# Optimization experiments

Hardware: AMD Instinct MI355X
Metric: run time of the kernel (lower is better)

The kernel has to match this reference:

```python
import jax, jax.numpy as jnp
import numpy as np
from jax import lax

GAMMA = 1.0
BIG = 1e8  # matches the torch init value 100000000.0


def setup_inputs() -> dict:
    key = jax.random.key(0)
    k1, k2 = jax.random.split(key)
    B, n, m, d = 256, 256, 256, 32
    x = jax.random.normal(k1, (B, n, d), dtype=jnp.float32)
    y = jax.random.normal(k2, (B, m, d), dtype=jnp.float32)
    return {"x": x, "y": y}


def _soft_dtw(x, y, gamma):
    B, n, d = x.shape
    m = y.shape[1]
    # squared euclidean distances, (B, n, m); GEMM form avoids the (B,n,m,d) blowup
    x2 = jnp.sum(x * x, axis=-1)
    y2 = jnp.sum(y * y, axis=-1)
    dist = x2[:, :, None] + y2[:, None, :] - 2.0 * jnp.einsum('bnd,bmd->bnm', x, y)
    dist = jnp.maximum(dist, 0.0)  # cdist(p=2)**2 is nonnegative

    def softmin3(a, b, c):
        s = jnp.stack([a, b, c], axis=0)
        return -gamma * jax.nn.logsumexp(-s / gamma, axis=0)

    big_col = jnp.full((B,), BIG, dtype=x.dtype)

    def row_step(prev_row, d_row):
        # prev_row: (B, m+1) = D[i-1, :];  d_row: (B, m) = dist[:, i-1, :]
        def col_step(cur, inp):
            # cur: (B,) = D[i, j-1]; inp: (dist[i-1,j-1], D[i-1,j], D[i-1,j-1])
            dij, up, diag = inp
            new = dij + softmin3(up, cur, diag)
            return new, new
        xs = (d_row.T, prev_row[:, 1:].T, prev_row[:, :-1].T)  # each (m, B)
        _, vals = lax.scan(col_step, big_col, xs)  # vals: (m, B)
        new_row = jnp.concatenate([big_col[:, None], vals.T], axis=1)  # (B, m+1)
        return new_row, None

    init_row = jnp.concatenate(
        [jnp.zeros((B, 1), x.dtype), jnp.full((B, m), BIG, dtype=x.dtype)], axis=1)
    final_row, _ = lax.scan(row_step, init_row, jnp.swapaxes(dist, 0, 1))  # scan over n rows
    return jnp.mean(final_row[:, m])


def reference(x, y):
    return _soft_dtw(x, y, GAMMA)
```

## Files before the change

### kernel.cpp

```cpp
#include <hip/hip_runtime.h>

#define BIG 1e8f
#define LN2 0.69314718f
#define LOG2E 1.44269504f
#define M2L -2.8853900818f

#define RSLOT 112
#define DRB 1040

#define OFF_XH   116480
#define OFF_X2S  132864
#define OFF_Y2S  133888
#define OFF_RDY  134912
#define OFF_PRG  134976
#define LDS_BYTES 135040

typedef _Float16 half8 __attribute__((ext_vector_type(8)));
typedef _Float16 half2_t __attribute__((ext_vector_type(2)));
typedef float f32x4 __attribute__((ext_vector_type(4)));

__device__ __forceinline__ float exp2g(float x) {
#if __has_builtin(__builtin_amdgcn_exp2f)
    return __builtin_amdgcn_exp2f(x);
#else
    return exp2f(x);
#endif
}
__device__ __forceinline__ float log2g(float x) {
#if __has_builtin(__builtin_amdgcn_logf)
    return __builtin_amdgcn_logf(x);
#else
    return log2f(x);
#endif
}

__device__ __forceinline__ half2_t pkrtz(float a, float b) {
    return __builtin_bit_cast(half2_t, __builtin_amdgcn_cvt_pkrtz(a, b));
}

__device__ __forceinline__ void pairp(float a, float b, float& m, float& s) {
    m = fminf(a, b);
    s = exp2g(-fabsf(a - b)) + 1.f;
}
__device__ __forceinline__ float smp(float m, float s, float v) {
    float d = v - m;
    float t = exp2g(-fabsf(d));
    float r = (d > 0.f) ? (t + s) : fmaf(s, t, 1.f);
    return fminf(m, v) - log2g(r);
}

__device__ __forceinline__ float shfl_up1(float v, float oldv) {
    int r = __builtin_amdgcn_update_dpp(
        __builtin_bit_cast(int, oldv), __builtin_bit_cast(int, v),
        0x138 , 0xf, 0xf, false);
    return __builtin_bit_cast(float, r);
}

__device__ __forceinline__ void dec2(unsigned int w, float& a, float& b) {
    half2_t h = __builtin_bit_cast(half2_t, w);
    a = (float)h[0];
    b = (float)h[1];
}

__global__ __launch_bounds__(128, 1) void sdtw_kernel(
    const float* __restrict__ x, const float* __restrict__ y,
    float* __restrict__ out) {
    extern __shared__ __align__(16) char smem[];
    unsigned char* band = (unsigned char*)smem;
    _Float16* xh = (_Float16*)(smem + OFF_XH);
    float* x2sL = (float*)(smem + OFF_X2S);
    float* y2sL = (float*)(smem + OFF_Y2S);
    volatile int* rdy = (volatile int*)(smem + OFF_RDY);
    volatile int* prg = (volatile int*)(smem + OFF_PRG);

    const int tid = threadIdx.x;
    const int b = blockIdx.x;
    const float* xb = x + (size_t)b * 8192;
    const float* yb = y + (size_t)b * 8192;

#pragma unroll
    for (int rr = 0; rr < 2; rr++) {
        const int r = tid + rr * 128;
        const float4* px = (const float4*)(xb + r * 32);
        union { _Float16 h[32]; half8 v[4]; } uc;
        float s2 = 0.f;
#pragma unroll
        for (int q = 0; q < 8; q++) {
            float4 f = px[q];
            s2 += f.x * f.x + f.y * f.y + f.z * f.z + f.w * f.w;
            uc.h[4 * q + 0] = (_Float16)f.x;
            uc.h[4 * q + 1] = (_Float16)f.y;
            uc.h[4 * q + 2] = (_Float16)f.z;
            uc.h[4 * q + 3] = (_Float16)f.w;
        }
        half8* dst = (half8*)&xh[r * 32];
#pragma unroll
        for (int q = 0; q < 4; q++) dst[q] = uc.v[q];
        x2sL[r] = s2 * LOG2E;

        const float4* py = (const float4*)(yb + r * 32);
        float t2 = 0.f;
#pragma unroll
        for (int q = 0; q < 8; q++) {
            float4 f = py[q];
            t2 += f.x * f.x + f.y * f.y + f.z * f.z + f.w * f.w;
        }
        y2sL[r] = t2 * LOG2E;
    }
    if (tid < 16) rdy[tid] = 0;
    if (tid == 16) *prg = 0;
    __syncthreads();

    if (tid >= 64) {
        const int lane = tid - 64;
        const int qd = lane >> 4, xr = lane & 15;

        half8 yfrag[16];
        float yvL[16];
#pragma unroll
        for (int ci = 0; ci < 16; ci++) {
            const float* yp = yb + (ci * 16 + xr) * 32 + qd * 8;
            float4 f0 = *(const float4*)yp;
            float4 f1 = *(const float4*)(yp + 4);
            half8 v;
            v[0] = (_Float16)f0.x; v[1] = (_Float16)f0.y;
            v[2] = (_Float16)f0.z; v[3] = (_Float16)f0.w;
            v[4] = (_Float16)f1.x; v[5] = (_Float16)f1.y;
            v[6] = (_Float16)f1.z; v[7] = (_Float16)f1.w;
            yfrag[ci] = v;
            yvL[ci] = y2sL[ci * 16 + xr];
        }

        for (int sg = 0; sg < 16; sg++) {
            if (sg >= 6) {
                const int need = 8 * sg - 40;
                while (*prg < need) {}
            }
            const half8 xf = *(const half8*)&xh[(sg * 16 + xr) * 32 + qd * 8];
            const float4 xl = *(const float4*)&x2sL[sg * 16 + qd * 4];
            const int p0 = 8 * sg + 2 * qd;
#pragma unroll
            for (int ci = 0; ci < 16; ci++) {
                f32x4 acc = {0.f, 0.f, 0.f, 0.f};
                acc = __builtin_amdgcn_mfma_f32_16x16x32_f16(xf, yfrag[ci], acc, 0, 0, 0);
                const int c = ci * 16 + xr;
                const float yv = yvL[ci];
                const float d0 = fmaxf(fmaf(M2L, acc[0], xl.x + yv), 0.f);
                const float d1 = fmaxf(fmaf(M2L, acc[1], xl.y + yv), 0.f);
                const float d2 = fmaxf(fmaf(M2L, acc[2], xl.z + yv), 0.f);
                const float d3 = fmaxf(fmaf(M2L, acc[3], xl.w + yv), 0.f);
                const half2_t h01 = pkrtz(d0, d1);
                const half2_t h23 = pkrtz(d2, d3);
                const int dr0 = p0 + (c >> 2);
                int s0_ = dr0;     if (s0_ >= RSLOT) s0_ -= RSLOT;
                int s1_ = dr0 + 1; if (s1_ >= RSLOT) s1_ -= RSLOT;
                *(half2_t*)&band[s0_ * DRB + 4 * c] = h01;
                *(half2_t*)&band[s1_ * DRB + 4 * c] = h23;
            }
            __threadfence_block();
            if (lane == 0) rdy[sg] = 1;
        }
        return;
    }

    const int lane = tid;
    float u0 = BIG, u1 = BIG, u2 = BIG, u3 = BIG, pA3 = BIG, pB3 = BIG;
    float G0 = (lane == 0) ? 0.f : BIG;
    float m0, s0, m1, s1, m2, s2, m3, s3;
    pairp(u0, G0, m0, s0);
    pairp(u1, u0, m1, s1);
    pairp(u2, u1, m2, s2);
    pairp(u3, u2, m3, s3);

    while (rdy[0] == 0) {}
    uint4 wreg = *(const uint4*)&band[16 * lane];

    for (int s_ = 1; s_ <= 191; s_++) {
        const float L0 = shfl_up1(pA3, BIG);
        const float L1 = shfl_up1(pB3, BIG);

        float dA0, dB0, dA1, dB1, dA2, dB2, dA3, dB3;
        dec2(wreg.x, dA0, dB0);
        dec2(wreg.y, dA1, dB1);
        dec2(wreg.z, dA2, dB2);
        dec2(wreg.w, dA3, dB3);

        const float A0 = dA0 + smp(m0, s0, L0);
        const float A1 = dA1 + smp(m1, s1, A0);
        const float A2 = dA2 + smp(m2, s2, A1);
        const float A3 = dA3 + smp(m3, s3, A2);

        if ((s_ & 7) == 0) {
            int st = s_ >> 3;
            if (st > 15) st = 15;
            while (rdy[st] == 0) {}
            if (lane == 0) *prg = s_;
        }
        int dn = (s_ > 190) ? 190 : s_;
        if (dn >= RSLOT) dn -= RSLOT;
        const uint4 wnext = *(const uint4*)&band[dn * DRB + 16 * lane];

        float n0, t0, n1, t1, n2, t2, n3, t3;
        pairp(A0, L0, n0, t0);
        pairp(A1, A0, n1, t1);
        pairp(A2, A1, n2, t2);
        pairp(A3, A2, n3, t3);
        const float B0 = dB0 + smp(n0, t0, L1);
        const float B1 = dB1 + smp(n1, t1, B0);
        const float B2 = dB2 + smp(n2, t2, B1);
        const float B3 = dB3 + smp(n3, t3, B2);

        const bool act = (unsigned)(s_ - lane - 1) < 128u;
        u0 = act ? B0 : u0;
        u1 = act ? B1 : u1;
        u2 = act ? B2 : u2;
        u3 = act ? B3 : u3;
        pA3 = act ? A3 : pA3;
        pB3 = act ? B3 : pB3;
        G0 = L1;
        pairp(u0, G0, m0, s0);
        pairp(u1, u0, m1, s1);
        pairp(u2, u1, m2, s2);
        pairp(u3, u2, m3, s3);
        wreg = wnext;
    }

    if (lane == 63) atomicAdd(out, u3 * (LN2 / 256.f));
}

extern "C" void kernel_launch(void* const* d_in, const int* in_sizes, int n_in,
                              void* d_out, int out_size, void* d_ws, size_t ws_size,
                              hipStream_t stream) {
    const float* x = (const float*)d_in[0];
    const float* y = (const float*)d_in[1];
    float* out = (float*)d_out;
    const int B = in_sizes[0] / (256 * 32);

    (void)hipFuncSetAttribute((const void*)sdtw_kernel,
                              hipFuncAttributeMaxDynamicSharedMemorySize,
                              LDS_BYTES);
    (void)hipMemsetAsync(d_out, 0, sizeof(float), stream);
    sdtw_kernel<<<dim3(B), dim3(128), LDS_BYTES, stream>>>(x, y, out);
}
```

Baseline: 136.8 us.

## Carry cell values as unnormalized (max, sum) pairs to drop logs from serial chain

```diff
diff --git a/kernel.cpp b/kernel.cpp
--- a/kernel.cpp
+++ b/kernel.cpp
@@ -38,15 +38,27 @@
     return __builtin_bit_cast(half2_t, __builtin_amdgcn_cvt_pkrtz(a, b));
 }
 
-__device__ __forceinline__ void pairp(float a, float b, float& m, float& s) {
-    m = fminf(a, b);
-    s = exp2g(-fabsf(a - b)) + 1.f;
-}
-__device__ __forceinline__ float smp(float m, float s, float v) {
-    float d = v - m;
-    float t = exp2g(-fabsf(d));
-    float r = (d > 0.f) ? (t + s) : fmaf(s, t, 1.f);
-    return fminf(m, v) - log2g(r);
+
+__device__ __forceinline__ void pmerge(float Ma, float Sa, float Mb, float Sb,
+                                       float& Mo, float& So) {
+    const float d = Ma - Mb;
+    const float e = exp2g(-fabsf(d));
+    Mo = fminf(Ma, Mb);
+    So = (d <= 0.f) ? fmaf(Sb, e, Sa) : fmaf(Sa, e, Sb);
+}
+
+__device__ __forceinline__ void pairp2(float a, float b, float& Mo, float& So) {
+    Mo = fminf(a, b);
+    So = exp2g(-fabsf(a - b)) + 1.f;
+}
+
+__device__ __forceinline__ void pcell(float Mm, float Sm, float Mv, float Sv,
+                                      float dd, float& Mo, float& So) {
+    const float dlt = Mv - Mm;
+    const float e = exp2g(-fabsf(dlt));
+    const float mu = fminf(Mm, Mv);
+    So = (dlt >= 0.f) ? fmaf(Sv, e, Sm) : fmaf(Sm, e, Sv);
+    Mo = dd + mu;
 }
 
 __device__ __forceinline__ float shfl_up1(float v, float oldv) {
@@ -164,20 +176,23 @@
     }
 
     const int lane = tid;
-    float u0 = BIG, u1 = BIG, u2 = BIG, u3 = BIG, pA3 = BIG, pB3 = BIG;
-    float G0 = (lane == 0) ? 0.f : BIG;
-    float m0, s0, m1, s1, m2, s2, m3, s3;
-    pairp(u0, G0, m0, s0);
-    pairp(u1, u0, m1, s1);
-    pairp(u2, u1, m2, s2);
-    pairp(u3, u2, m3, s3);
+    float aU0 = BIG, aU1 = BIG, aU2 = BIG, aU3 = BIG;
+    float MpA3 = BIG, SpA3 = 1.f, MpB3 = BIG, SpB3 = 1.f;
+    float MG0 = (lane == 0) ? 0.f : BIG, SG0 = 1.f;
+    float Mm0, Sm0, Mm1, Sm1, Mm2, Sm2, Mm3, Sm3;
+    pmerge(aU0, 1.f, MG0, SG0, Mm0, Sm0);
+    pairp2(aU1, aU0, Mm1, Sm1);
+    pairp2(aU2, aU1, Mm2, Sm2);
+    pairp2(aU3, aU2, Mm3, Sm3);
 
     while (rdy[0] == 0) {}
     uint4 wreg = *(const uint4*)&band[16 * lane];
 
     for (int s_ = 1; s_ <= 191; s_++) {
-        const float L0 = shfl_up1(pA3, BIG);
-        const float L1 = shfl_up1(pB3, BIG);
+        const float MLA = shfl_up1(MpA3, BIG);
+        const float SLA = shfl_up1(SpA3, 1.f);
+        const float MLB = shfl_up1(MpB3, BIG);
+        const float SLB = shfl_up1(SpB3, 1.f);
 
         float dA0, dB0, dA1, dB1, dA2, dB2, dA3, dB3;
         dec2(wreg.x, dA0, dB0);
@@ -185,10 +200,11 @@
         dec2(wreg.z, dA2, dB2);
         dec2(wreg.w, dA3, dB3);
 
-        const float A0 = dA0 + smp(m0, s0, L0);
-        const float A1 = dA1 + smp(m1, s1, A0);
-        const float A2 = dA2 + smp(m2, s2, A1);
-        const float A3 = dA3 + smp(m3, s3, A2);
+        float MA0, SA0, MA1, SA1, MA2, SA2, MA3, SA3;
+        pcell(Mm0, Sm0, MLA, SLA, dA0, MA0, SA0);
+        pcell(Mm1, Sm1, MA0, SA0, dA1, MA1, SA1);
+        pcell(Mm2, Sm2, MA1, SA1, dA2, MA2, SA2);
+        pcell(Mm3, Sm3, MA2, SA2, dA3, MA3, SA3);
 
         if ((s_ & 7) == 0) {
             int st = s_ >> 3;
@@ -200,32 +216,38 @@
         if (dn >= RSLOT) dn -= RSLOT;
         const uint4 wnext = *(const uint4*)&band[dn * DRB + 16 * lane];
 
-        float n0, t0, n1, t1, n2, t2, n3, t3;
-        pairp(A0, L0, n0, t0);
-        pairp(A1, A0, n1, t1);
-        pairp(A2, A1, n2, t2);
-        pairp(A3, A2, n3, t3);
-        const float B0 = dB0 + smp(n0, t0, L1);
-        const float B1 = dB1 + smp(n1, t1, B0);
-        const float B2 = dB2 + smp(n2, t2, B1);
-        const float B3 = dB3 + smp(n3, t3, B2);
+        float Mn0, Sn0, Mn1, Sn1, Mn2, Sn2, Mn3, Sn3;
+        pmerge(MA0, SA0, MLA, SLA, Mn0, Sn0);
+        pmerge(MA1, SA1, MA0, SA0, Mn1, Sn1);
+        pmerge(MA2, SA2, MA1, SA1, Mn2, Sn2);
+        pmerge(MA3, SA3, MA2, SA2, Mn3, Sn3);
+        float MB0, SB0, MB1, SB1, MB2, SB2, MB3, SB3;
+        pcell(Mn0, Sn0, MLB, SLB, dB0, MB0, SB0);
+        pcell(Mn1, Sn1, MB0, SB0, dB1, MB1, SB1);
+        pcell(Mn2, Sn2, MB1, SB1, dB2, MB2, SB2);
+        pcell(Mn3, Sn3, MB2, SB2, dB3, MB3, SB3);
+
+        const float aB0 = MB0 - log2g(SB0);
+        const float aB1 = MB1 - log2g(SB1);
+        const float aB2 = MB2 - log2g(SB2);
+        const float aB3 = MB3 - log2g(SB3);
 
         const bool act = (unsigned)(s_ - lane - 1) < 128u;
-        u0 = act ? B0 : u0;
-        u1 = act ? B1 : u1;
-        u2 = act ? B2 : u2;
-        u3 = act ? B3 : u3;
-        pA3 = act ? A3 : pA3;
-        pB3 = act ? B3 : pB3;
-        G0 = L1;
-        pairp(u0, G0, m0, s0);
-        pairp(u1, u0, m1, s1);
-        pairp(u2, u1, m2, s2);
-        pairp(u3, u2, m3, s3);
+        aU0 = act ? aB0 : aU0;
+        aU1 = act ? aB1 : aU1;
+        aU2 = act ? aB2 : aU2;
+        aU3 = act ? aB3 : aU3;
+        MpA3 = act ? MA3 : MpA3; SpA3 = act ? SA3 : SpA3;
+        MpB3 = act ? MB3 : MpB3; SpB3 = act ? SB3 : SpB3;
+        MG0 = MLB; SG0 = SLB;
+        pmerge(aU0, 1.f, MG0, SG0, Mm0, Sm0);
+        pairp2(aU1, aU0, Mm1, Sm1);
+        pairp2(aU2, aU1, Mm2, Sm2);
+        pairp2(aU3, aU2, Mm3, Sm3);
         wreg = wnext;
     }
 
-    if (lane == 63) atomicAdd(out, u3 * (LN2 / 256.f));
+    if (lane == 63) atomicAdd(out, aU3 * (LN2 / 256.f));
 }
 
 extern "C" void kernel_launch(void* const* d_in, const int* in_sizes, int n_in,
```

Result: no change. 138.3 us (+1.1%).
